# Optimization experiments

Hardware: AMD Instinct MI355X
Metric: run time of the kernel (lower is better)

Reference implementation:

```python
import jax, jax.numpy as jnp
import numpy as np

B, C, E = 4, 2048, 1024
H = 16
HD = E // H  # 64

def setup_inputs() -> dict:
    key = jax.random.key(0)
    k1, k2, k3 = jax.random.split(key, 3)
    x = jax.random.normal(k1, (B, C, E), dtype=jnp.float32)
    W_attn = jax.random.normal(k2, (E, 3 * E), dtype=jnp.float32) * 0.02
    W_proj = jax.random.normal(k3, (E, E), dtype=jnp.float32) * 0.02
    return {"x": x, "W_attn": W_attn, "W_proj": W_proj}

def reference(x, W_attn, W_proj):
    b, c, e = x.shape
    qkv = x @ W_attn                      # [B,C,3E]
    q, k, v = jnp.split(qkv, 3, axis=-1)
    # [B,C,E] -> [B,H,C,HD]
    q = q.reshape(b, c, H, HD).transpose(0, 2, 1, 3)
    k = k.reshape(b, c, H, HD).transpose(0, 2, 1, 3)
    v = v.reshape(b, c, H, HD).transpose(0, 2, 1, 3)
    scale = 1.0 / np.sqrt(HD).astype(np.float32)
    att = jnp.einsum('bhqd,bhkd->bhqk', q, k) * scale  # [B,H,C,C]
    causal = jnp.tril(jnp.ones((c, c), dtype=bool))
    att = jnp.where(causal[None, None, :, :], att, -jnp.inf)
    att = jax.nn.softmax(att, axis=-1)
    y = jnp.einsum('bhqk,bhkd->bhqd', att, v)          # [B,H,C,HD]
    y = y.transpose(0, 2, 1, 3).reshape(b, c, e)
    return y @ W_proj
```

## Files before the change

### kernel.cpp

```cpp
#include <hip/hip_runtime.h>
#include <hip/hip_bf16.h>


typedef unsigned short ushort_t;
typedef __attribute__((ext_vector_type(8))) short short8;
typedef __attribute__((ext_vector_type(4))) float floatx4;
typedef __attribute__((ext_vector_type(16))) float floatx16;

#define NH   16
#define SEQ  2048
#define EMB  1024
#define HDIM 64

#define MFMA32(a, b, c) __builtin_amdgcn_mfma_f32_32x32x16_bf16(a, b, c, 0, 0, 0)

__device__ __forceinline__ ushort_t f2bf(float f) {
    union { float f; unsigned u; } v; v.f = f;
    unsigned r = (v.u + 0x7fffu + ((v.u >> 16) & 1u)) >> 16;
    return (ushort_t)r;
}

#if defined(__has_builtin) && __has_builtin(__builtin_amdgcn_global_load_lds)
#define HAS_GLL 1
__device__ __forceinline__ void gload16(const ushort_t* g, ushort_t* l) {
    __builtin_amdgcn_global_load_lds((const __attribute__((address_space(1))) void*)g,
                                     (__attribute__((address_space(3))) void*)l, 16, 0, 0);
}
#else
#define HAS_GLL 0
#endif

__global__ __launch_bounds__(256) void cast_k(const float* __restrict__ in,
                                              ushort_t* __restrict__ out) {
    int i = blockIdx.x * 256 + threadIdx.x;
    float4 v0 = ((const float4*)in)[i * 2];
    float4 v1 = ((const float4*)in)[i * 2 + 1];
    short8 t;
    t[0] = (short)f2bf(v0.x); t[1] = (short)f2bf(v0.y);
    t[2] = (short)f2bf(v0.z); t[3] = (short)f2bf(v0.w);
    t[4] = (short)f2bf(v1.x); t[5] = (short)f2bf(v1.y);
    t[6] = (short)f2bf(v1.z); t[7] = (short)f2bf(v1.w);
    ((short8*)out)[i] = t;
}

__global__ void transpose_cast_k(const float* __restrict__ in, ushort_t* __restrict__ out,
                                 int R, int Cc) {
    __shared__ ushort_t tile[32][33];
    int x  = blockIdx.x * 32 + threadIdx.x;
    int y0 = blockIdx.y * 32;
#pragma unroll
    for (int i = 0; i < 32; i += 8)
        tile[threadIdx.y + i][threadIdx.x] = f2bf(in[(size_t)(y0 + threadIdx.y + i) * Cc + x]);
    __syncthreads();
    int xo = blockIdx.y * 32 + threadIdx.x;
    int yo = blockIdx.x * 32;
#pragma unroll
    for (int i = 0; i < 32; i += 8)
        out[(size_t)(yo + threadIdx.y + i) * R + xo] = tile[threadIdx.x][threadIdx.y + i];
}

__global__ void transpose_v_k(const ushort_t* __restrict__ in, ushort_t* __restrict__ out) {
    __shared__ ushort_t tile[32][33];
    int bh = blockIdx.z;
    int c0 = blockIdx.x * 32, d0 = blockIdx.y * 32;
#pragma unroll
    for (int i = 0; i < 32; i += 8)
        tile[threadIdx.y + i][threadIdx.x] =
            in[((size_t)bh * SEQ + c0 + threadIdx.y + i) * HDIM + d0 + threadIdx.x];
    __syncthreads();
#pragma unroll
    for (int i = 0; i < 32; i += 8)
        out[((size_t)bh * HDIM + d0 + threadIdx.y + i) * SEQ + c0 + threadIdx.x] =
            tile[threadIdx.x][threadIdx.y + i];
}

template<int EPI>
__global__ __launch_bounds__(256) void gemm_bt(const ushort_t* __restrict__ A,
                                               const ushort_t* __restrict__ Bt,
                                               void* __restrict__ O0v,
                                               ushort_t* __restrict__ O1,
                                               ushort_t* __restrict__ O2,
                                               int M, int N, int K) {
    __shared__ __align__(16) ushort_t As[128 * 64];
    __shared__ __align__(16) ushort_t Bs[128 * 64];
    const int tid  = threadIdx.x;
    const int wv   = tid >> 6, lane = tid & 63, quad = lane >> 4, l15 = lane & 15;
    const int wm   = wv >> 1, wn = wv & 1;
    const int bm   = blockIdx.x, bn = blockIdx.y;
    const int lrow = lane >> 3;
    const int kg   = (lane & 7) ^ (lrow & 7);
    const int sw   = l15 & 7;

    floatx4 acc[4][4];
#pragma unroll
    for (int i = 0; i < 4; i++)
#pragma unroll
        for (int j = 0; j < 4; j++) acc[i][j] = (floatx4){0.f, 0.f, 0.f, 0.f};

    for (int kt = 0; kt < K; kt += 64) {
#pragma unroll
        for (int it = 0; it < 4; it++) {
            int r0 = it * 32 + wv * 8;
            const ushort_t* ga = &A [(size_t)(bm * 128 + r0 + lrow) * K + kt + kg * 8];
            const ushort_t* gb = &Bt[(size_t)(bn * 128 + r0 + lrow) * K + kt + kg * 8];
#if HAS_GLL
            gload16(ga, &As[r0 * 64]);
            gload16(gb, &Bs[r0 * 64]);
#else
            *(uint4*)&As[(r0 + lrow) * 64 + (lane & 7) * 8] = *(const uint4*)ga;
            *(uint4*)&Bs[(r0 + lrow) * 64 + (lane & 7) * 8] = *(const uint4*)gb;
#endif
        }
        __syncthreads();
#pragma unroll
        for (int ks = 0; ks < 2; ks++) {
            short8 af[4], bf[4];
#pragma unroll
            for (int i = 0; i < 4; i++)
                af[i] = *(const short8*)&As[(wm * 64 + i * 16 + l15) * 64 + (((ks * 4 + quad) ^ sw) * 8)];
#pragma unroll
            for (int j = 0; j < 4; j++)
                bf[j] = *(const short8*)&Bs[(wn * 64 + j * 16 + l15) * 64 + (((ks * 4 + quad) ^ sw) * 8)];
#pragma unroll
            for (int i = 0; i < 4; i++)
#pragma unroll
                for (int j = 0; j < 4; j++)
                    acc[i][j] = __builtin_amdgcn_mfma_f32_16x16x32_bf16(af[i], bf[j], acc[i][j], 0, 0, 0);
        }
        __syncthreads();
    }

#pragma unroll
    for (int i = 0; i < 4; i++)
#pragma unroll
        for (int j = 0; j < 4; j++)
#pragma unroll
            for (int r = 0; r < 4; r++) {
                int row = bm * 128 + wm * 64 + i * 16 + quad * 4 + r;
                int col = bn * 128 + wn * 64 + j * 16 + l15;
                if (EPI == 0) {
                    ((float*)O0v)[(size_t)row * N + col] = acc[i][j][r];
                } else {
                    ushort_t v = f2bf(acc[i][j][r]);
                    int b = row >> 11, c = row & 2047;
                    int which = col >> 10, nn = col & 1023;
                    int hh = nn >> 6, d = nn & 63;
                    ushort_t* dst = (which == 0) ? (ushort_t*)O0v : (which == 1) ? O1 : O2;
                    dst[((size_t)(b * NH + hh) * SEQ + c) * HDIM + d] = v;
                }
            }
}

__global__ __launch_bounds__(256) void attn3_k(const ushort_t* __restrict__ Qg,
                                               const ushort_t* __restrict__ Kg,
                                               const ushort_t* __restrict__ Vtg,
                                               ushort_t* __restrict__ Y) {
    __shared__ __align__(16) ushort_t Ks[64 * 64];
    __shared__ __align__(16) ushort_t Vs[64 * 64];
    __shared__ __align__(16) ushort_t Ps[4][32 * 64];
    const int tid  = threadIdx.x;
    const int wv   = tid >> 6, lane = tid & 63;
    const int l31  = lane & 31, hf = lane >> 5;
    const int z    = blockIdx.x, bh = blockIdx.y;
    const int qs7  = l31 & 7;
    const int lrow = lane >> 3;
    const int kgs  = (lane & 7) ^ (lrow & 7);
    ushort_t* Pw = Ps[wv];
    const int b = bh >> 4, hh = bh & 15;
    const float c2 = 0.18033688011112042f;

    for (int pp = 0; pp < 2; pp++) {
        const int qb = pp ? (15 - z) : z;
        const int qrow0 = qb * 128 + wv * 32;
        const int q_abs = qrow0 + l31;
        const int jmax_w = 2 * qb + (wv >> 1);
        const int jmax_b = 2 * qb + 1;

        short8 qf[4];
        {
            const ushort_t* qp = Qg + ((size_t)bh * SEQ + q_abs) * HDIM + hf * 8;
#pragma unroll
            for (int ks = 0; ks < 4; ks++) qf[ks] = *(const short8*)(qp + ks * 16);
        }

        floatx16 o0, o1;
#pragma unroll
        for (int r = 0; r < 16; r++) { o0[r] = 0.f; o1[r] = 0.f; }
        float m_i = -1e30f, l_i = 0.f;

        for (int j = 0; j <= jmax_b; j++) {
#pragma unroll
            for (int it = 0; it < 2; it++) {
                int r0 = it * 32 + wv * 8;
                const ushort_t* gk = &Kg [((size_t)bh * SEQ  + j * 64 + r0 + lrow) * HDIM + kgs * 8];
                const ushort_t* gv = &Vtg[((size_t)bh * HDIM + r0 + lrow) * SEQ + j * 64 + kgs * 8];
#if HAS_GLL
                gload16(gk, &Ks[r0 * 64]);
                gload16(gv, &Vs[r0 * 64]);
#else
                *(uint4*)&Ks[(r0 + lrow) * 64 + (lane & 7) * 8] = *(const uint4*)gk;
                *(uint4*)&Vs[(r0 + lrow) * 64 + (lane & 7) * 8] = *(const uint4*)gv;
#endif
            }
            __syncthreads();

            if (j <= jmax_w) {
                floatx16 s0, s1;
#pragma unroll
                for (int r = 0; r < 16; r++) { s0[r] = 0.f; s1[r] = 0.f; }
#pragma unroll
                for (int ks = 0; ks < 4; ks++) {
                    int slot = ((hf + 2 * ks) ^ qs7) * 8;
                    short8 k0 = *(const short8*)&Ks[l31 * 64 + slot];
                    short8 k1 = *(const short8*)&Ks[(32 + l31) * 64 + slot];
                    s0 = MFMA32(k0, qf[ks], s0);
                    s1 = MFMA32(k1, qf[ks], s1);
                }

                if (j == jmax_w) {
                    const int kb0 = j * 64 + 4 * hf;
#pragma unroll
                    for (int r = 0; r < 16; r++) {
                        int key = kb0 + (r & 3) + 8 * (r >> 2);
                        s0[r] = (key > q_abs) ? -1e30f : s0[r] * c2;
                        s1[r] = (key + 32 > q_abs) ? -1e30f : s1[r] * c2;
                    }
                } else {
#pragma unroll
                    for (int r = 0; r < 16; r++) { s0[r] *= c2; s1[r] *= c2; }
                }

                float mx = -1e30f;
#pragma unroll
                for (int r = 0; r < 16; r++) mx = fmaxf(mx, fmaxf(s0[r], s1[r]));
                mx = fmaxf(mx, __shfl_xor(mx, 32));
                float m_new = fmaxf(m_i, mx);
                float alpha = __builtin_amdgcn_exp2f(m_i - m_new);
                m_i = m_new;

                float rs = 0.f;
#pragma unroll
                for (int r = 0; r < 16; r++) {
                    s0[r] = __builtin_amdgcn_exp2f(s0[r] - m_new);
                    s1[r] = __builtin_amdgcn_exp2f(s1[r] - m_new);
                    rs += s0[r] + s1[r];
                }
                rs += __shfl_xor(rs, 32);
                l_i = l_i * alpha + rs;

#pragma unroll
                for (int g = 0; g < 4; g++) {
                    uint2 w0, w1;
                    w0.x = (unsigned)f2bf(s0[g * 4])     | ((unsigned)f2bf(s0[g * 4 + 1]) << 16);
                    w0.y = (unsigned)f2bf(s0[g * 4 + 2]) | ((unsigned)f2bf(s0[g * 4 + 3]) << 16);
                    w1.x = (unsigned)f2bf(s1[g * 4])     | ((unsigned)f2bf(s1[g * 4 + 1]) << 16);
                    w1.y = (unsigned)f2bf(s1[g * 4 + 2]) | ((unsigned)f2bf(s1[g * 4 + 3]) << 16);
                    *(uint2*)&Pw[l31 * 64 + ((g     ^ qs7) * 8) + 4 * hf] = w0;
                    *(uint2*)&Pw[l31 * 64 + (((4+g) ^ qs7) * 8) + 4 * hf] = w1;
                }

#pragma unroll
                for (int r = 0; r < 16; r++) { o0[r] *= alpha; o1[r] *= alpha; }

#pragma unroll
                for (int ks = 0; ks < 4; ks++) {
                    int slot = ((hf + 2 * ks) ^ qs7) * 8;
                    short8 v0 = *(const short8*)&Vs[l31 * 64 + slot];
                    short8 v1 = *(const short8*)&Vs[(32 + l31) * 64 + slot];
                    short8 pf = *(const short8*)&Pw[l31 * 64 + (((ks * 2 + hf) ^ qs7) * 8)];
                    o0 = MFMA32(v0, pf, o0);
                    o1 = MFMA32(v1, pf, o1);
                }
            }
            __syncthreads();
        }

        float inv = 1.0f / l_i;
#pragma unroll
        for (int g = 0; g < 4; g++) {
            uint2 w0, w1;
            w0.x = (unsigned)f2bf(o0[g * 4] * inv)     | ((unsigned)f2bf(o0[g * 4 + 1] * inv) << 16);
            w0.y = (unsigned)f2bf(o0[g * 4 + 2] * inv) | ((unsigned)f2bf(o0[g * 4 + 3] * inv) << 16);
            w1.x = (unsigned)f2bf(o1[g * 4] * inv)     | ((unsigned)f2bf(o1[g * 4 + 1] * inv) << 16);
            w1.y = (unsigned)f2bf(o1[g * 4 + 2] * inv) | ((unsigned)f2bf(o1[g * 4 + 3] * inv) << 16);
            *(uint2*)&Pw[l31 * 64 + ((g     ^ qs7) * 8) + 4 * hf] = w0;
            *(uint2*)&Pw[l31 * 64 + (((4+g) ^ qs7) * 8) + 4 * hf] = w1;
        }
        const int dg = lane & 7;
#pragma unroll
        for (int sb = 0; sb < 4; sb++) {
            int ql = sb * 8 + (lane >> 3);
            uint4 v = *(const uint4*)&Pw[ql * 64 + ((dg ^ (ql & 7)) * 8)];
            *(uint4*)&Y[((size_t)(b * SEQ + qrow0 + ql)) * EMB + hh * HDIM + dg * 8] = v;
        }
    }
}

extern "C" void kernel_launch(void* const* d_in, const int* in_sizes, int n_in,
                              void* d_out, int out_size, void* d_ws, size_t ws_size,
                              hipStream_t stream) {
    const float* x      = (const float*)d_in[0];
    const float* W_attn = (const float*)d_in[1];
    const float* W_proj = (const float*)d_in[2];

    char* ws = (char*)d_ws;
    ushort_t* Wt_attn = (ushort_t*)(ws);
    ushort_t* Wt_proj = (ushort_t*)(ws + 6291456);
    ushort_t* Xb      = (ushort_t*)(ws + 8388608);
    ushort_t* Vt      = Xb;
    ushort_t* Qb      = (ushort_t*)(ws + 25165824);
    ushort_t* Kb      = (ushort_t*)(ws + 41943040);
    ushort_t* Vb      = (ushort_t*)(ws + 58720256);
    ushort_t* Yb      = Vb;

    cast_k<<<4096, 256, 0, stream>>>(x, Xb);
    transpose_cast_k<<<dim3(3072 / 32, 1024 / 32), dim3(32, 8), 0, stream>>>(W_attn, Wt_attn, 1024, 3072);
    transpose_cast_k<<<dim3(1024 / 32, 1024 / 32), dim3(32, 8), 0, stream>>>(W_proj, Wt_proj, 1024, 1024);
    gemm_bt<1><<<dim3(8192 / 128, 3072 / 128), 256, 0, stream>>>(Xb, Wt_attn, Qb, Kb, Vb, 8192, 3072, 1024);
    transpose_v_k<<<dim3(SEQ / 32, HDIM / 32, 64), dim3(32, 8), 0, stream>>>(Vb, Vt);
    attn3_k<<<dim3(8, 64), 256, 0, stream>>>(Qb, Kb, Vt, Yb);
    gemm_bt<0><<<dim3(8192 / 128, 1024 / 128), 256, 0, stream>>>(Yb, Wt_proj, d_out,
                                                                 nullptr, nullptr, 8192, 1024, 1024);
}
```

Measured before the change: 267.7 us.

## Double-buffer K/V tiles, pass P via lane shuffles, one query block per workgroup

The attention kernel now double-buffers the K and V tiles in LDS, prefetching tile j+1 while tile j is computed, which drops one barrier per iteration. The P matrix goes from registers into the PV MFMA through cross-half shuffles instead of an LDS round trip. The alpha rescale is skipped when no row maximum grows, and bf16 packing uses the hardware convert instruction. The grid moves from 8 workgroups, each handling a pair of short and long query blocks, to 16 workgroups with one block each, launched heaviest first. This gives up the explicit causal load balancing in exchange for more parallelism.

```diff
diff --git a/kernel.cpp b/kernel.cpp
--- a/kernel.cpp
+++ b/kernel.cpp
@@ -18,6 +18,19 @@
     union { float f; unsigned u; } v; v.f = f;
     unsigned r = (v.u + 0x7fffu + ((v.u >> 16) & 1u)) >> 16;
     return (ushort_t)r;
+}
+
+__device__ __forceinline__ unsigned pkbf(float a, float b) {
+#if defined(__has_builtin) && __has_builtin(__builtin_amdgcn_cvt_pk_bf16_f32)
+    auto r = __builtin_amdgcn_cvt_pk_bf16_f32(a, b);
+    unsigned u; __builtin_memcpy(&u, &r, 4);
+    return u;
+#else
+    float2 t; t.x = a; t.y = b;
+    __hip_bfloat162 h = __float22bfloat162_rn(t);
+    unsigned u; __builtin_memcpy(&u, &h, 4);
+    return u;
+#endif
 }
 
 #if defined(__has_builtin) && __has_builtin(__builtin_amdgcn_global_load_lds)
@@ -151,148 +164,171 @@
             }
 }
 
-__global__ __launch_bounds__(256) void attn3_k(const ushort_t* __restrict__ Qg,
+__device__ __forceinline__ void stage_tiles(const ushort_t* __restrict__ Kg,
+                                            const ushort_t* __restrict__ Vtg,
+                                            ushort_t* Ksb, ushort_t* Vsb,
+                                            int bh, int j, int wv, int lrow, int kgs, int lane) {
+#pragma unroll
+    for (int it = 0; it < 2; it++) {
+        int r0 = it * 32 + wv * 8;
+        const ushort_t* gk = &Kg [((size_t)bh * SEQ  + j * 64 + r0 + lrow) * HDIM + kgs * 8];
+        const ushort_t* gv = &Vtg[((size_t)bh * HDIM + r0 + lrow) * SEQ + j * 64 + kgs * 8];
+#if HAS_GLL
+        gload16(gk, &Ksb[r0 * 64]);
+        gload16(gv, &Vsb[r0 * 64]);
+#else
+        *(uint4*)&Ksb[(r0 + lrow) * 64 + (lane & 7) * 8] = *(const uint4*)gk;
+        *(uint4*)&Vsb[(r0 + lrow) * 64 + (lane & 7) * 8] = *(const uint4*)gv;
+#endif
+    }
+}
+
+__global__ __launch_bounds__(256) void attn4_k(const ushort_t* __restrict__ Qg,
                                                const ushort_t* __restrict__ Kg,
                                                const ushort_t* __restrict__ Vtg,
                                                ushort_t* __restrict__ Y) {
-    __shared__ __align__(16) ushort_t Ks[64 * 64];
-    __shared__ __align__(16) ushort_t Vs[64 * 64];
-    __shared__ __align__(16) ushort_t Ps[4][32 * 64];
+    __shared__ __align__(16) ushort_t Ks[2][64 * 64];
+    __shared__ __align__(16) ushort_t Vs[2][64 * 64];
     const int tid  = threadIdx.x;
     const int wv   = tid >> 6, lane = tid & 63;
     const int l31  = lane & 31, hf = lane >> 5;
-    const int z    = blockIdx.x, bh = blockIdx.y;
+    const int qb   = 15 - blockIdx.x, bh = blockIdx.y;
     const int qs7  = l31 & 7;
     const int lrow = lane >> 3;
     const int kgs  = (lane & 7) ^ (lrow & 7);
-    ushort_t* Pw = Ps[wv];
     const int b = bh >> 4, hh = bh & 15;
     const float c2 = 0.18033688011112042f;
-
-    for (int pp = 0; pp < 2; pp++) {
-        const int qb = pp ? (15 - z) : z;
-        const int qrow0 = qb * 128 + wv * 32;
-        const int q_abs = qrow0 + l31;
-        const int jmax_w = 2 * qb + (wv >> 1);
-        const int jmax_b = 2 * qb + 1;
-
-        short8 qf[4];
-        {
-            const ushort_t* qp = Qg + ((size_t)bh * SEQ + q_abs) * HDIM + hf * 8;
-#pragma unroll
-            for (int ks = 0; ks < 4; ks++) qf[ks] = *(const short8*)(qp + ks * 16);
+    const int qrow0 = qb * 128 + wv * 32;
+    const int q_abs = qrow0 + l31;
+    const int jmax_b = 2 * qb + 1;
+    const int jmax_w = 2 * qb + (wv >> 1);
+
+    short8 qf[4];
+    {
+        const ushort_t* qp = Qg + ((size_t)bh * SEQ + q_abs) * HDIM + hf * 8;
+#pragma unroll
+        for (int ks = 0; ks < 4; ks++) qf[ks] = *(const short8*)(qp + ks * 16);
+    }
+
+    floatx16 o0, o1;
+#pragma unroll
+    for (int r = 0; r < 16; r++) { o0[r] = 0.f; o1[r] = 0.f; }
+    float m_i = -1e30f, l_i = 0.f;
+
+    stage_tiles(Kg, Vtg, Ks[0], Vs[0], bh, 0, wv, lrow, kgs, lane);
+
+    for (int j = 0; j <= jmax_b; j++) {
+        const int cur = j & 1;
+        __syncthreads();
+        if (j < jmax_b)
+            stage_tiles(Kg, Vtg, Ks[cur ^ 1], Vs[cur ^ 1], bh, j + 1, wv, lrow, kgs, lane);
+
+        if (j <= jmax_w) {
+            floatx16 s0, s1;
+#pragma unroll
+            for (int r = 0; r < 16; r++) { s0[r] = 0.f; s1[r] = 0.f; }
+#pragma unroll
+            for (int ks = 0; ks < 4; ks++) {
+                int slot = ((hf + 2 * ks) ^ qs7) * 8;
+                short8 k0 = *(const short8*)&Ks[cur][l31 * 64 + slot];
+                short8 k1 = *(const short8*)&Ks[cur][(32 + l31) * 64 + slot];
+                s0 = MFMA32(k0, qf[ks], s0);
+                s1 = MFMA32(k1, qf[ks], s1);
+            }
+
+            short8 vf0[4], vf1[4];
+#pragma unroll
+            for (int ks = 0; ks < 4; ks++) {
+                int slot = ((hf + 2 * ks) ^ qs7) * 8;
+                vf0[ks] = *(const short8*)&Vs[cur][l31 * 64 + slot];
+                vf1[ks] = *(const short8*)&Vs[cur][(32 + l31) * 64 + slot];
+            }
+
+            if (j == jmax_w) {
+                const int kb0 = j * 64 + 4 * hf;
+#pragma unroll
+                for (int r = 0; r < 16; r++) {
+                    int key = kb0 + (r & 3) + 8 * (r >> 2);
+                    s0[r] = (key > q_abs) ? -1e30f : s0[r] * c2;
+                    s1[r] = (key + 32 > q_abs) ? -1e30f : s1[r] * c2;
+                }
+            } else {
+#pragma unroll
+                for (int r = 0; r < 16; r++) { s0[r] *= c2; s1[r] *= c2; }
+            }
+
+            float mx = -1e30f;
+#pragma unroll
+            for (int r = 0; r < 16; r++) mx = fmaxf(mx, fmaxf(s0[r], s1[r]));
+            mx = fmaxf(mx, __shfl_xor(mx, 32));
+            const bool need = __any(mx > m_i);
+            float m_new = fmaxf(m_i, mx);
+            float alpha = need ? __builtin_amdgcn_exp2f(m_i - m_new) : 1.0f;
+            m_i = m_new;
+
+            float rs = 0.f;
+#pragma unroll
+            for (int r = 0; r < 16; r++) {
+                s0[r] = __builtin_amdgcn_exp2f(s0[r] - m_new);
+                s1[r] = __builtin_amdgcn_exp2f(s1[r] - m_new);
+                rs += s0[r] + s1[r];
+            }
+            rs += __shfl_xor(rs, 32);
+            l_i = l_i * alpha + rs;
+
+            uint2 pk[8];
+#pragma unroll
+            for (int g = 0; g < 4; g++) {
+                pk[g].x     = pkbf(s0[g * 4],     s0[g * 4 + 1]);
+                pk[g].y     = pkbf(s0[g * 4 + 2], s0[g * 4 + 3]);
+                pk[4 + g].x = pkbf(s1[g * 4],     s1[g * 4 + 1]);
+                pk[4 + g].y = pkbf(s1[g * 4 + 2], s1[g * 4 + 3]);
+            }
+
+            if (need) {
+#pragma unroll
+                for (int r = 0; r < 16; r++) { o0[r] *= alpha; o1[r] *= alpha; }
+            }
+
+#pragma unroll
+            for (int ks = 0; ks < 4; ks++) {
+                int bi = 4 * (ks >> 1) + 2 * (ks & 1);
+                uint2 own  = pk[bi + hf];
+                uint2 send = pk[bi + (hf ^ 1)];
+                uint2 oth;
+                oth.x = (unsigned)__shfl_xor((int)send.x, 32);
+                oth.y = (unsigned)__shfl_xor((int)send.y, 32);
+                union { short8 s; uint4 u; } pf;
+                pf.u.x = hf ? oth.x : own.x;
+                pf.u.y = hf ? oth.y : own.y;
+                pf.u.z = hf ? own.x : oth.x;
+                pf.u.w = hf ? own.y : oth.y;
+                o0 = MFMA32(vf0[ks], pf.s, o0);
+                o1 = MFMA32(vf1[ks], pf.s, o1);
+            }
         }
-
-        floatx16 o0, o1;
-#pragma unroll
-        for (int r = 0; r < 16; r++) { o0[r] = 0.f; o1[r] = 0.f; }
-        float m_i = -1e30f, l_i = 0.f;
-
-        for (int j = 0; j <= jmax_b; j++) {
-#pragma unroll
-            for (int it = 0; it < 2; it++) {
-                int r0 = it * 32 + wv * 8;
-                const ushort_t* gk = &Kg [((size_t)bh * SEQ  + j * 64 + r0 + lrow) * HDIM + kgs * 8];
-                const ushort_t* gv = &Vtg[((size_t)bh * HDIM + r0 + lrow) * SEQ + j * 64 + kgs * 8];
-#if HAS_GLL
-                gload16(gk, &Ks[r0 * 64]);
-                gload16(gv, &Vs[r0 * 64]);
-#else
-                *(uint4*)&Ks[(r0 + lrow) * 64 + (lane & 7) * 8] = *(const uint4*)gk;
-                *(uint4*)&Vs[(r0 + lrow) * 64 + (lane & 7) * 8] = *(const uint4*)gv;
-#endif
-            }
-            __syncthreads();
-
-            if (j <= jmax_w) {
-                floatx16 s0, s1;
-#pragma unroll
-                for (int r = 0; r < 16; r++) { s0[r] = 0.f; s1[r] = 0.f; }
-#pragma unroll
-                for (int ks = 0; ks < 4; ks++) {
-                    int slot = ((hf + 2 * ks) ^ qs7) * 8;
-                    short8 k0 = *(const short8*)&Ks[l31 * 64 + slot];
-                    short8 k1 = *(const short8*)&Ks[(32 + l31) * 64 + slot];
-                    s0 = MFMA32(k0, qf[ks], s0);
-                    s1 = MFMA32(k1, qf[ks], s1);
-                }
-
-                if (j == jmax_w) {
-                    const int kb0 = j * 64 + 4 * hf;
-#pragma unroll
-                    for (int r = 0; r < 16; r++) {
-                        int key = kb0 + (r & 3) + 8 * (r >> 2);
-                        s0[r] = (key > q_abs) ? -1e30f : s0[r] * c2;
-                        s1[r] = (key + 32 > q_abs) ? -1e30f : s1[r] * c2;
-                    }
-                } else {
-#pragma unroll
-                    for (int r = 0; r < 16; r++) { s0[r] *= c2; s1[r] *= c2; }
-                }
-
-                float mx = -1e30f;
-#pragma unroll
-                for (int r = 0; r < 16; r++) mx = fmaxf(mx, fmaxf(s0[r], s1[r]));
-                mx = fmaxf(mx, __shfl_xor(mx, 32));
-                float m_new = fmaxf(m_i, mx);
-                float alpha = __builtin_amdgcn_exp2f(m_i - m_new);
-                m_i = m_new;
-
-                float rs = 0.f;
-#pragma unroll
-                for (int r = 0; r < 16; r++) {
-                    s0[r] = __builtin_amdgcn_exp2f(s0[r] - m_new);
-                    s1[r] = __builtin_amdgcn_exp2f(s1[r] - m_new);
-                    rs += s0[r] + s1[r];
-                }
-                rs += __shfl_xor(rs, 32);
-                l_i = l_i * alpha + rs;
-
-#pragma unroll
-                for (int g = 0; g < 4; g++) {
-                    uint2 w0, w1;
-                    w0.x = (unsigned)f2bf(s0[g * 4])     | ((unsigned)f2bf(s0[g * 4 + 1]) << 16);
-                    w0.y = (unsigned)f2bf(s0[g * 4 + 2]) | ((unsigned)f2bf(s0[g * 4 + 3]) << 16);
-                    w1.x = (unsigned)f2bf(s1[g * 4])     | ((unsigned)f2bf(s1[g * 4 + 1]) << 16);
-                    w1.y = (unsigned)f2bf(s1[g * 4 + 2]) | ((unsigned)f2bf(s1[g * 4 + 3]) << 16);
-                    *(uint2*)&Pw[l31 * 64 + ((g     ^ qs7) * 8) + 4 * hf] = w0;
-                    *(uint2*)&Pw[l31 * 64 + (((4+g) ^ qs7) * 8) + 4 * hf] = w1;
-                }
-
-#pragma unroll
-                for (int r = 0; r < 16; r++) { o0[r] *= alpha; o1[r] *= alpha; }
-
-#pragma unroll
-                for (int ks = 0; ks < 4; ks++) {
-                    int slot = ((hf + 2 * ks) ^ qs7) * 8;
-                    short8 v0 = *(const short8*)&Vs[l31 * 64 + slot];
-                    short8 v1 = *(const short8*)&Vs[(32 + l31) * 64 + slot];
-                    short8 pf = *(const short8*)&Pw[l31 * 64 + (((ks * 2 + hf) ^ qs7) * 8)];
-                    o0 = MFMA32(v0, pf, o0);
-                    o1 = MFMA32(v1, pf, o1);
-                }
-            }
-            __syncthreads();
-        }
-
-        float inv = 1.0f / l_i;
-#pragma unroll
-        for (int g = 0; g < 4; g++) {
-            uint2 w0, w1;
-            w0.x = (unsigned)f2bf(o0[g * 4] * inv)     | ((unsigned)f2bf(o0[g * 4 + 1] * inv) << 16);
-            w0.y = (unsigned)f2bf(o0[g * 4 + 2] * inv) | ((unsigned)f2bf(o0[g * 4 + 3] * inv) << 16);
-            w1.x = (unsigned)f2bf(o1[g * 4] * inv)     | ((unsigned)f2bf(o1[g * 4 + 1] * inv) << 16);
-            w1.y = (unsigned)f2bf(o1[g * 4 + 2] * inv) | ((unsigned)f2bf(o1[g * 4 + 3] * inv) << 16);
-            *(uint2*)&Pw[l31 * 64 + ((g     ^ qs7) * 8) + 4 * hf] = w0;
-            *(uint2*)&Pw[l31 * 64 + (((4+g) ^ qs7) * 8) + 4 * hf] = w1;
-        }
-        const int dg = lane & 7;
-#pragma unroll
-        for (int sb = 0; sb < 4; sb++) {
-            int ql = sb * 8 + (lane >> 3);
-            uint4 v = *(const uint4*)&Pw[ql * 64 + ((dg ^ (ql & 7)) * 8)];
-            *(uint4*)&Y[((size_t)(b * SEQ + qrow0 + ql)) * EMB + hh * HDIM + dg * 8] = v;
-        }
+    }
+
+    __syncthreads();
+    ushort_t* Ew = &Ks[0][0] + wv * 2048;
+    float inv = 1.0f / l_i;
+#pragma unroll
+    for (int g = 0; g < 4; g++) {
+        uint2 w0, w1;
+        w0.x = pkbf(o0[g * 4] * inv,     o0[g * 4 + 1] * inv);
+        w0.y = pkbf(o0[g * 4 + 2] * inv, o0[g * 4 + 3] * inv);
+        w1.x = pkbf(o1[g * 4] * inv,     o1[g * 4 + 1] * inv);
+        w1.y = pkbf(o1[g * 4 + 2] * inv, o1[g * 4 + 3] * inv);
+        *(uint2*)&Ew[l31 * 64 + ((g     ^ qs7) * 8) + 4 * hf] = w0;
+        *(uint2*)&Ew[l31 * 64 + (((4+g) ^ qs7) * 8) + 4 * hf] = w1;
+    }
+    __builtin_amdgcn_s_waitcnt(0);
+    const int dg = lane & 7;
+#pragma unroll
+    for (int sb = 0; sb < 4; sb++) {
+        int ql = sb * 8 + (lane >> 3);
+        uint4 v = *(const uint4*)&Ew[ql * 64 + ((dg ^ (ql & 7)) * 8)];
+        *(uint4*)&Y[((size_t)(b * SEQ + qrow0 + ql)) * EMB + hh * HDIM + dg * 8] = v;
     }
 }
 
@@ -318,7 +354,7 @@
     transpose_cast_k<<<dim3(1024 / 32, 1024 / 32), dim3(32, 8), 0, stream>>>(W_proj, Wt_proj, 1024, 1024);
     gemm_bt<1><<<dim3(8192 / 128, 3072 / 128), 256, 0, stream>>>(Xb, Wt_attn, Qb, Kb, Vb, 8192, 3072, 1024);
     transpose_v_k<<<dim3(SEQ / 32, HDIM / 32, 64), dim3(32, 8), 0, stream>>>(Vb, Vt);
-    attn3_k<<<dim3(8, 64), 256, 0, stream>>>(Qb, Kb, Vt, Yb);
+    attn4_k<<<dim3(16, 64), 256, 0, stream>>>(Qb, Kb, Vt, Yb);
     gemm_bt<0><<<dim3(8192 / 128, 1024 / 128), 256, 0, stream>>>(Yb, Wt_proj, d_out,
                                                                  nullptr, nullptr, 8192, 1024, 1024);
 }
```

Result: slower. 384.1 us (+43.5%).
